# Kernel tuning notes

Hardware: AMD Instinct MI355X
Metric: run time of the kernel (lower is better)

Reference implementation:

```python
import jax, jax.numpy as jnp
import numpy as np

# Mamba2 defaults (mamba_ssm): d_state=128, d_conv=4, expand=2, headdim=64, ngroups=1
NB, D_MODEL, D_STATE, D_CONV, HEADDIM = 2, 512, 128, 4, 64
D_INNER = 2 * D_MODEL                      # expand * d_model
NHEADS = D_INNER // HEADDIM                # 16
CONV_DIM = D_INNER + 2 * D_STATE           # x, B, C go through depthwise conv
D_IN_PROJ = 2 * D_INNER + 2 * D_STATE + NHEADS  # z, xBC, dt
VOCAB, LABEL, B, L = 32000, 1000, 2, 512


def setup_inputs() -> dict:
    key = jax.random.key(0)
    ks = jax.random.split(key, 8)
    nrm = lambda k, shape, s: jax.random.normal(k, shape, dtype=jnp.float32) * s
    tokens = jax.random.randint(ks[0], (B, L), 0, VOCAB)
    embedding = nrm(ks[1], (VOCAB, D_MODEL), 0.02)
    in_proj_w = nrm(ks[2], (NB, D_IN_PROJ, D_MODEL), D_MODEL ** -0.5)
    conv_w = nrm(ks[3], (NB, CONV_DIM, D_CONV), D_CONV ** -0.5)
    conv_b = jnp.zeros((NB, CONV_DIM), jnp.float32)
    # dt_bias = inverse-softplus of dt ~ logUniform[1e-3, 0.1] (Mamba2 init)
    dt = jnp.exp(jax.random.uniform(ks[4], (NB, NHEADS), minval=float(np.log(1e-3)), maxval=float(np.log(0.1))))
    dt_bias = dt + jnp.log(-jnp.expm1(-dt))
    A_log = jnp.log(jax.random.uniform(ks[5], (NB, NHEADS), minval=1.0, maxval=16.0))
    D = jnp.ones((NB, NHEADS), jnp.float32)
    rms_w = jnp.ones((NB, D_INNER), jnp.float32)
    out_proj_w = nrm(ks[6], (NB, D_MODEL, D_INNER), D_INNER ** -0.5)
    ln_w = jnp.ones((NB, D_MODEL), jnp.float32)
    ln_b = jnp.zeros((NB, D_MODEL), jnp.float32)
    head_w = nrm(ks[7], (LABEL, D_MODEL), D_MODEL ** -0.5)
    head_b = jnp.zeros((LABEL,), jnp.float32)
    return dict(tokens=tokens, embedding=embedding, in_proj_w=in_proj_w, conv_w=conv_w,
                conv_b=conv_b, dt_bias=dt_bias, A_log=A_log, D=D, rms_w=rms_w,
                out_proj_w=out_proj_w, ln_w=ln_w, ln_b=ln_b, head_w=head_w, head_b=head_b)


def _mamba2(u, Wi, cw, cb, dtb, Alog, Dv, rw, Wo):
    b, l, _ = u.shape
    zxbcdt = u @ Wi.T                                  # (b,l,D_IN_PROJ)
    z = zxbcdt[..., :D_INNER]
    xBC = zxbcdt[..., D_INNER:D_INNER + CONV_DIM]
    dt = jax.nn.softplus(zxbcdt[..., D_INNER + CONV_DIM:] + dtb)   # (b,l,h)
    # causal depthwise conv1d, kernel size D_CONV
    xp = jnp.pad(xBC, ((0, 0), (D_CONV - 1, 0), (0, 0)))
    xBC = sum(xp[:, k:k + l, :] * cw[:, k] for k in range(D_CONV)) + cb
    xBC = jax.nn.silu(xBC)
    xh = xBC[..., :D_INNER].reshape(b, l, NHEADS, HEADDIM)
    Bm = xBC[..., D_INNER:D_INNER + D_STATE]           # (b,l,n), ngroups=1
    Cm = xBC[..., D_INNER + D_STATE:]                  # (b,l,n)
    A = -jnp.exp(Alog)                                 # (h,)
    dA = jnp.exp(dt * A)                               # (b,l,h)

    def step(h, inp):
        dA_t, dt_t, x_t, B_t, C_t = inp                # (b,h),(b,h),(b,h,p),(b,n),(b,n)
        h = h * dA_t[:, :, None, None] + (dt_t[:, :, None] * x_t)[..., None] * B_t[:, None, None, :]
        return h, jnp.einsum('bhpn,bn->bhp', h, C_t)

    h0 = jnp.zeros((b, NHEADS, HEADDIM, D_STATE), u.dtype)
    inp = (jnp.swapaxes(dA, 0, 1), jnp.swapaxes(dt, 0, 1), jnp.swapaxes(xh, 0, 1),
           jnp.swapaxes(Bm, 0, 1), jnp.swapaxes(Cm, 0, 1))
    _, ys = jax.lax.scan(step, h0, inp)
    y = jnp.swapaxes(ys, 0, 1) + Dv[:, None] * xh      # (b,l,h,p)
    # gated RMSNorm (norm_before_gate=False): normalize y*silu(z)
    y = y.reshape(b, l, D_INNER) * jax.nn.silu(z)
    y = y * jax.lax.rsqrt(jnp.mean(y * y, -1, keepdims=True) + 1e-5) * rw
    return y @ Wo.T


def _layernorm(x, w, bias):
    mu = jnp.mean(x, -1, keepdims=True)
    xc = x - mu
    var = jnp.mean(xc * xc, -1, keepdims=True)
    return xc * jax.lax.rsqrt(var + 1e-5) * w + bias


def reference(tokens, embedding, in_proj_w, conv_w, conv_b, dt_bias, A_log, D,
              rms_w, out_proj_w, ln_w, ln_b, head_w, head_b):
    x = embedding[tokens]                              # (b,l,d)
    for i in range(NB):
        y = _mamba2(x, in_proj_w[i], conv_w[i], conv_b[i], dt_bias[i],
                    A_log[i], D[i], rms_w[i], out_proj_w[i])
        x = _layernorm(y + x, ln_w[i], ln_b[i])        # residual + LN (dropout=identity)
    return x @ head_w.T + head_b                        # (b,l,label)
```

## Files before the change

kernel.cpp:

```cpp
#include <hip/hip_runtime.h>

#define L_SEQ 512
#define BATCH 2
#define NROWS (BATCH*L_SEQ)
#define DMODEL 512
#define DINNER 1024
#define DSTATE 128
#define NHEADSM 16
#define CONVD 1280
#define DINPROJ 2320
#define QCH 32
#define NCH 16
#define WI_PAD 2368
#define WH_PAD 1024

#define W_CONVW 0
#define W_CONVB 10240
#define W_DTB   12800
#define W_ALOG  12832
#define W_DD    12864
#define W_RMSW  12896
#define W_LNW   14944
#define W_LNB   15968
#define W_HEADB 16992
#define O_X     18048
#define O_ZX    (O_X  + NROWS*DMODEL)
#define O_XC    (O_ZX + NROWS*DINPROJ)
#define O_DT    (O_XC + NROWS*CONVD)
#define O_Y     (O_DT + NROWS*NHEADSM)
#define O_O     (O_Y  + NROWS*DINNER)
#define O_LA    (O_O  + NROWS*DMODEL)
#define O_S     (O_LA + 16384)
#define O_UB    (O_S  + 4194304)
#define U_WI   0
#define U_WO   2424832
#define U_WH   3473408
#define U_XBF  3997696
#define U_YBF  4521984

#define NPREPW (2*WI_PAD + 2*DMODEL + WH_PAD)

typedef __attribute__((ext_vector_type(8))) short short8;
typedef __attribute__((ext_vector_type(4))) float floatx4;

__device__ __forceinline__ float b2f(unsigned short h){ return __uint_as_float(((unsigned)h)<<16); }
__device__ __forceinline__ unsigned short f2b(float x){
  unsigned u = __float_as_uint(x);
  return (unsigned short)((u + 0x7fffu + ((u>>16)&1u)) >> 16);
}
__device__ __forceinline__ float loadIn(const void* p, long i, int f){
  return f ? b2f(((const unsigned short*)p)[i]) : ((const float*)p)[i];
}
__device__ __forceinline__ float silu(float s){ return s / (1.f + __expf(-s)); }

struct ConvArgs { const void* src[9]; int off[10]; };

__global__ void k_prep(ConvArgs a, const void* __restrict__ wi, const void* __restrict__ wo,
                       const void* __restrict__ wh, const int* __restrict__ tok,
                       const void* __restrict__ emb, int* __restrict__ flagOut,
                       float* __restrict__ dstSmall,
                       unsigned short* __restrict__ WiB, unsigned short* __restrict__ WoB,
                       unsigned short* __restrict__ WhB,
                       float* __restrict__ x, unsigned short* __restrict__ xbf)
{
  __shared__ int sflag;
  int t = threadIdx.x;
  if (t < 64){
    int cnt = 0;
    #pragma unroll 8
    for (int i = 0; i < 64; i++){
      unsigned w0 = ((const unsigned*)emb)[t + 64*i];
      unsigned e = (w0 >> 7) & 0xffu;
      cnt += (e >= 100 && e <= 126) ? 1 : 0;
    }
    #pragma unroll
    for (int o = 1; o < 64; o <<= 1) cnt += __shfl_xor(cnt, o);
    if (t == 0) sflag = (cnt > 2048) ? 1 : 0;
  }
  __syncthreads();
  int f = sflag;
  if (blockIdx.x == 0 && t == 0) *flagOut = f;

  int blk = blockIdx.x;
  if (blk < 71){
    int i = blk*256 + t;
    if (i < a.off[9]){
      int s = 0;
      while (i >= a.off[s+1]) s++;
      dstSmall[i] = loadIn(a.src[s], i - a.off[s], f);
    }
    return;
  }
  blk -= 71;
  if (blk < NPREPW){
    int r = blk;
    const void* src = nullptr; unsigned short* dst; long sb = 0, db; int K; bool zero = false;
    if (r < 2*WI_PAD){
      int layer = r / WI_PAD, row = r % WI_PAD;
      K = DMODEL; dst = WiB; db = ((long)layer*WI_PAD + row)*DMODEL;
      if (row < DINPROJ){ src = wi; sb = ((long)layer*DINPROJ + row)*DMODEL; } else zero = true;
    } else if (r < 2*WI_PAD + 2*DMODEL){
      int rr = r - 2*WI_PAD;
      K = DINNER; dst = WoB; db = (long)rr*DINNER;
      src = wo; sb = db;
    } else {
      int row = r - 2*WI_PAD - 2*DMODEL;
      K = DMODEL; dst = WhB; db = (long)row*DMODEL;
      if (row < 1000){ src = wh; sb = db; } else zero = true;
    }
    for (int c = t; c < K; c += 256)
      dst[db + c] = zero ? (unsigned short)0
                         : (f ? ((const unsigned short*)src)[sb + c] : f2b(((const float*)src)[sb + c]));
    return;
  }
  int r = blk - NPREPW;
  long base = (long)tok[r] * DMODEL;
  for (int c = t; c < DMODEL; c += 256){
    float v = loadIn(emb, base + c, f);
    x[(long)r*DMODEL + c] = v;
    xbf[(long)r*DMODEL + c] = f ? ((const unsigned short*)emb)[base + c] : f2b(v);
  }
}

__global__ __launch_bounds__(256) void k_mfma_nt(
    const unsigned short* __restrict__ A, const unsigned short* __restrict__ B,
    void* __restrict__ C, int M, int N, int K,
    const float* __restrict__ bias, const int* __restrict__ flag, int outDual)
{
  __shared__ unsigned short As[4096];
  __shared__ unsigned short Bs[4096];
  int t = threadIdx.x;
  int w = t >> 6, lane = t & 63;
  int quad = lane >> 4, l16 = lane & 15;
  int m0 = blockIdx.y << 6, n0 = blockIdx.x << 6;
  int wm = (w & 1) << 5, wn = (w >> 1) << 5;
  floatx4 acc[2][2];
  #pragma unroll
  for (int mi = 0; mi < 2; mi++)
    #pragma unroll
    for (int ni = 0; ni < 2; ni++) acc[mi][ni] = (floatx4){0.f,0.f,0.f,0.f};

  int idx0 = (w << 7) + lane;
  int r0s = idx0 >> 3, g0 = idx0 & 7;
  int idx1 = idx0 + 64;
  int r1s = idx1 >> 3, g1 = idx1 & 7;
  long aOff0 = (long)(m0 + r0s)*K + g0*8;
  long aOff1 = (long)(m0 + r1s)*K + g1*8;
  long bOff0 = (long)(n0 + r0s)*K + g0*8;
  long bOff1 = (long)(n0 + r1s)*K + g1*8;
  int w0 = r0s*64 + (g0 ^ (r0s & 7))*8;
  int w1 = r1s*64 + (g1 ^ (r1s & 7))*8;

  for (int k0 = 0; k0 < K; k0 += 64){
    short8 a0 = *(const short8*)&A[aOff0 + k0];
    short8 a1 = *(const short8*)&A[aOff1 + k0];
    short8 b0 = *(const short8*)&B[bOff0 + k0];
    short8 b1 = *(const short8*)&B[bOff1 + k0];
    __syncthreads();
    *(short8*)&As[w0] = a0; *(short8*)&As[w1] = a1;
    *(short8*)&Bs[w0] = b0; *(short8*)&Bs[w1] = b1;
    __syncthreads();
    #pragma unroll
    for (int ks = 0; ks < 2; ks++){
      short8 af[2], bfr[2];
      #pragma unroll
      for (int mi = 0; mi < 2; mi++){
        int r = wm + mi*16 + l16;
        int pos = ((ks << 2) + quad) ^ (r & 7);
        af[mi] = *(const short8*)&As[r*64 + pos*8];
      }
      #pragma unroll
      for (int ni = 0; ni < 2; ni++){
        int r = wn + ni*16 + l16;
        int pos = ((ks << 2) + quad) ^ (r & 7);
        bfr[ni] = *(const short8*)&Bs[r*64 + pos*8];
      }
      #pragma unroll
      for (int mi = 0; mi < 2; mi++)
        #pragma unroll
        for (int ni = 0; ni < 2; ni++)
          acc[mi][ni] = __builtin_amdgcn_mfma_f32_16x16x32_bf16(af[mi], bfr[ni], acc[mi][ni], 0, 0, 0);
    }
  }
  int f = *flag;
  #pragma unroll
  for (int mi = 0; mi < 2; mi++)
    #pragma unroll
    for (int ni = 0; ni < 2; ni++){
      int col = n0 + wn + ni*16 + l16;
      if (col >= N) continue;
      float bv = bias ? bias[col] : 0.f;
      #pragma unroll
      for (int rr = 0; rr < 4; rr++){
        int row = m0 + wm + mi*16 + (quad << 2) + rr;
        float v = acc[mi][ni][rr] + bv;
        long idx = (long)row*N + col;
        if (outDual && f) ((unsigned short*)C)[idx] = f2b(v);
        else              ((float*)C)[idx] = v;
      }
    }
}

__global__ __launch_bounds__(256) void k_conv_dt(
    const float* __restrict__ zx, const float* __restrict__ cw, const float* __restrict__ cb,
    const float* __restrict__ dtb, unsigned short* __restrict__ xcb, float* __restrict__ dt)
{
  int r = blockIdx.x; int b = r >> 9, l = r & 511;
  int t = threadIdx.x;
  for (int c = t; c < CONVD; c += 256){
    float s = cb[c];
    #pragma unroll
    for (int k = 0; k < 4; k++){
      int pos = l - 3 + k;
      if (pos >= 0)
        s = fmaf(zx[(long)(b*L_SEQ + pos)*DINPROJ + DINNER + c], cw[c*4 + k], s);
    }
    xcb[(long)r*CONVD + c] = f2b(silu(s));
  }
  if (t < NHEADSM){
    float v = zx[(long)r*DINPROJ + DINNER + CONVD + t] + dtb[t];
    dt[r*NHEADSM + t] = (v > 20.f) ? v : log1pf(__expf(v));
  }
}

__global__ __launch_bounds__(256) void k_chunk1(
    const unsigned short* __restrict__ xcb, const float* __restrict__ dtbuf,
    const float* __restrict__ alog, const float* __restrict__ dvec,
    float* __restrict__ S, float* __restrict__ LAb, float* __restrict__ y)
{
  int c = blockIdx.x, h = blockIdx.y, b = blockIdx.z;
  int t = threadIdx.x, w = t >> 6, lane = t & 63;
  int quad = lane >> 4, l16 = lane & 15;
  int l0 = c*QCH;
  __shared__ unsigned short XT[64*40];
  __shared__ unsigned short BTc[128*40];
  __shared__ unsigned short Bb[32*136];
  __shared__ unsigned short Cb[32*136];
  __shared__ unsigned short Gb[32*40];
  __shared__ float dtl[32], lal[32], coef[32];
  float A  = -__expf(alog[h]);
  float Dv = dvec[h];

  unsigned short xus[8];
  #pragma unroll
  for (int k = 0; k < 8; k++){
    int idx = t + k*256; int j = idx >> 6, p = idx & 63;
    xus[k] = xcb[(long)(b*L_SEQ + l0 + j)*CONVD + h*64 + p];
  }
  unsigned short bus[16], cus[16];
  #pragma unroll
  for (int k = 0; k < 16; k++){
    int idx = t + k*256; int j = idx >> 7, n = idx & 127;
    long rb = (long)(b*L_SEQ + l0 + j)*CONVD + DINNER;
    bus[k] = xcb[rb + n];
    cus[k] = xcb[rb + DSTATE + n];
  }
  if (t < 32) dtl[t] = dtbuf[(b*L_SEQ + l0 + t)*NHEADSM + h];
  __syncthreads();
  if (t == 0){ float s = 0.f; for (int i = 0; i < 32; i++){ s += dtl[i]; lal[i] = s*A; } }
  __syncthreads();
  if (t < 32){
    coef[t] = __expf(lal[31] - lal[t]) * dtl[t];
    LAb[(b*NHEADSM + h)*L_SEQ + l0 + t] = lal[t];
  }
  __syncthreads();
  #pragma unroll
  for (int k = 0; k < 8; k++){
    int idx = t + k*256; int j = idx >> 6, p = idx & 63;
    XT[p*40 + j] = xus[k];
  }
  #pragma unroll
  for (int k = 0; k < 16; k++){
    int idx = t + k*256; int j = idx >> 7, n = idx & 127;
    Bb[j*136 + n] = bus[k];
    Cb[j*136 + n] = cus[k];
    BTc[n*40 + j] = f2b(b2f(bus[k]) * coef[j]);
  }
  __syncthreads();

  short8 afS = *(const short8*)&XT[(w*16 + l16)*40 + quad*8];
  floatx4 accS[8];
  #pragma unroll
  for (int nb = 0; nb < 8; nb++){
    short8 bfS = *(const short8*)&BTc[(nb*16 + l16)*40 + quad*8];
    accS[nb] = __builtin_amdgcn_mfma_f32_16x16x32_bf16(afS, bfS, (floatx4){0.f,0.f,0.f,0.f}, 0, 0, 0);
  }
  int ti = w & 1, tj = w >> 1;
  floatx4 accG = (floatx4){0.f,0.f,0.f,0.f};
  #pragma unroll
  for (int ks = 0; ks < 4; ks++){
    short8 ga = *(const short8*)&Cb[(ti*16 + l16)*136 + ks*32 + quad*8];
    short8 gb = *(const short8*)&Bb[(tj*16 + l16)*136 + ks*32 + quad*8];
    accG = __builtin_amdgcn_mfma_f32_16x16x32_bf16(ga, gb, accG, 0, 0, 0);
  }
  long sb = ((long)((b*NHEADSM + h)*NCH + c))*8192;
  #pragma unroll
  for (int nb = 0; nb < 8; nb++)
    #pragma unroll
    for (int rr = 0; rr < 4; rr++)
      S[sb + (w*16 + quad*4 + rr)*128 + nb*16 + l16] = accS[nb][rr];
  #pragma unroll
  for (int rr = 0; rr < 4; rr++){
    int i = ti*16 + quad*4 + rr, j = tj*16 + l16;
    float g = (j <= i) ? __expf(lal[i] - lal[j]) * dtl[j] * accG[rr] : 0.f;
    Gb[i*40 + j] = f2b(g);
  }
  __syncthreads();
  short8 ag = *(const short8*)&Gb[(ti*16 + l16)*40 + quad*8];
  #pragma unroll
  for (int s = 0; s < 2; s++){
    int pb = (w >> 1)*2 + s;
    short8 bx = *(const short8*)&XT[(pb*16 + l16)*40 + quad*8];
    floatx4 accY = __builtin_amdgcn_mfma_f32_16x16x32_bf16(ag, bx, (floatx4){0.f,0.f,0.f,0.f}, 0, 0, 0);
    #pragma unroll
    for (int rr = 0; rr < 4; rr++){
      int i = ti*16 + quad*4 + rr, p = pb*16 + l16;
      float xval = b2f(XT[p*40 + i]);
      y[(long)(b*L_SEQ + l0 + i)*DINNER + h*64 + p] = fmaf(Dv, xval, accY[rr]);
    }
  }
}

__global__ __launch_bounds__(256) void k_chunk2(
    float* __restrict__ S, const float* __restrict__ LAb)
{
  int bh = blockIdx.x >> 5;
  int e = ((blockIdx.x & 31) << 8) + threadIdx.x;
  long base = (long)bh*NCH*8192 + e;
  int laBase = bh*L_SEQ;
  float lam[NCH];
  #pragma unroll
  for (int c = 0; c < NCH; c++) lam[c] = __expf(LAb[laBase + c*QCH + QCH - 1]);
  float hr = 0.f;
  #pragma unroll
  for (int c = 0; c < NCH; c++){
    long off = base + (long)c*8192;
    float sv = S[off];
    S[off] = hr;
    hr = fmaf(hr, lam[c], sv);
  }
}

__global__ __launch_bounds__(256) void k_chunk3(
    const unsigned short* __restrict__ xcb, const float* __restrict__ H,
    const float* __restrict__ LAb, float* __restrict__ y)
{
  int c = blockIdx.x, h = blockIdx.y, b = blockIdx.z;
  int t = threadIdx.x, w = t >> 6, lane = t & 63;
  int quad = lane >> 4, l16 = lane & 15;
  int l0 = c*QCH, bh = b*NHEADSM + h;
  __shared__ unsigned short Cb[32*136];
  __shared__ unsigned short Hhi[64*136];
  __shared__ unsigned short Hlo[64*136];
  __shared__ float el[32];
  if (t < 32) el[t] = __expf(LAb[bh*L_SEQ + l0 + t]);
  #pragma unroll
  for (int k = 0; k < 16; k++){
    int idx = t + k*256; int j = idx >> 7, n = idx & 127;
    Cb[j*136 + n] = xcb[(long)(b*L_SEQ + l0 + j)*CONVD + DINNER + DSTATE + n];
  }
  long hb = ((long)(bh*NCH + c))*8192;
  #pragma unroll
  for (int k = 0; k < 32; k++){
    int idx = t + k*256; int p = idx >> 7, n = idx & 127;
    float v = H[hb + idx];
    unsigned short hi = f2b(v);
    Hhi[p*136 + n] = hi;
    Hlo[p*136 + n] = f2b(v - b2f(hi));
  }
  __syncthreads();
  int ti = w & 1;
  #pragma unroll
  for (int s = 0; s < 2; s++){
    int pb = (w >> 1)*2 + s;
    floatx4 acc = (floatx4){0.f,0.f,0.f,0.f};
    #pragma unroll
    for (int ks = 0; ks < 4; ks++){
      short8 a  = *(const short8*)&Cb [(ti*16 + l16)*136 + ks*32 + quad*8];
      short8 bl = *(const short8*)&Hlo[(pb*16 + l16)*136 + ks*32 + quad*8];
      short8 bh2= *(const short8*)&Hhi[(pb*16 + l16)*136 + ks*32 + quad*8];
      acc = __builtin_amdgcn_mfma_f32_16x16x32_bf16(a, bl, acc, 0, 0, 0);
      acc = __builtin_amdgcn_mfma_f32_16x16x32_bf16(a, bh2, acc, 0, 0, 0);
    }
    #pragma unroll
    for (int rr = 0; rr < 4; rr++){
      int i = ti*16 + quad*4 + rr, p = pb*16 + l16;
      long yb = (long)(b*L_SEQ + l0 + i)*DINNER + h*64 + p;
      y[yb] = fmaf(el[i], acc[rr], y[yb]);
    }
  }
}

__global__ __launch_bounds__(256) void k_gated_rms(
    const float* __restrict__ y, const float* __restrict__ zx, const float* __restrict__ rw,
    unsigned short* __restrict__ ybf)
{
  int r = blockIdx.x, t = threadIdx.x;
  float g[4]; float ss = 0.f;
  #pragma unroll
  for (int i = 0; i < 4; i++){
    int c = t + i*256;
    float z  = zx[(long)r*DINPROJ + c];
    float yv = y[(long)r*DINNER + c];
    g[i] = yv * silu(z);
    ss = fmaf(g[i], g[i], ss);
  }
  #pragma unroll
  for (int o = 1; o < 64; o <<= 1) ss += __shfl_xor(ss, o);
  __shared__ float red[4];
  int w = t >> 6, lane = t & 63;
  if (lane == 0) red[w] = ss;
  __syncthreads();
  float tot = red[0] + red[1] + red[2] + red[3];
  float sc = rsqrtf(tot / (float)DINNER + 1e-5f);
  #pragma unroll
  for (int i = 0; i < 4; i++){
    int c = t + i*256;
    ybf[(long)r*DINNER + c] = f2b(g[i] * sc * rw[c]);
  }
}

__global__ __launch_bounds__(256) void k_add_ln(
    float* __restrict__ x, const float* __restrict__ o,
    const float* __restrict__ lw, const float* __restrict__ lb,
    unsigned short* __restrict__ xbf)
{
  int r = blockIdx.x, t = threadIdx.x;
  float v[2]; float sm = 0.f;
  #pragma unroll
  for (int i = 0; i < 2; i++){ int c = t + i*256; v[i] = x[(long)r*DMODEL + c] + o[(long)r*DMODEL + c]; sm += v[i]; }
  #pragma unroll
  for (int off = 1; off < 64; off <<= 1) sm += __shfl_xor(sm, off);
  __shared__ float red[4]; __shared__ float red2[4];
  int w = t >> 6, lane = t & 63;
  if (lane == 0) red[w] = sm;
  __syncthreads();
  float mu = (red[0] + red[1] + red[2] + red[3]) / (float)DMODEL;
  float var = 0.f;
  #pragma unroll
  for (int i = 0; i < 2; i++){ v[i] -= mu; var = fmaf(v[i], v[i], var); }
  #pragma unroll
  for (int off = 1; off < 64; off <<= 1) var += __shfl_xor(var, off);
  if (lane == 0) red2[w] = var;
  __syncthreads();
  float vv = (red2[0] + red2[1] + red2[2] + red2[3]) / (float)DMODEL;
  float sc = rsqrtf(vv + 1e-5f);
  #pragma unroll
  for (int i = 0; i < 2; i++){
    int c = t + i*256;
    float ov = v[i]*sc*lw[c] + lb[c];
    x[(long)r*DMODEL + c] = ov;
    xbf[(long)r*DMODEL + c] = f2b(ov);
  }
}

extern "C" void kernel_launch(void* const* d_in, const int* in_sizes, int n_in,
                              void* d_out, int out_size, void* d_ws, size_t ws_size,
                              hipStream_t stream)
{
  const int* tokens = (const int*)d_in[0];
  const void* emb = d_in[1];
  int* flag = (int*)d_ws;
  float* ws = (float*)((char*)d_ws + 256);

  ConvArgs ca;
  const int sizes[9] = {10240, 2560, 32, 32, 32, 2048, 1024, 1024, 1000};
  const int idxs[9]  = {3, 4, 5, 6, 7, 8, 10, 11, 13};
  int off = 0;
  for (int s = 0; s < 9; s++){ ca.src[s] = d_in[idxs[s]]; ca.off[s] = off; off += sizes[s]; }
  ca.off[9] = off;

  float* X  = ws + O_X;
  float* ZX = ws + O_ZX;
  float* DT = ws + O_DT;
  float* Y  = ws + O_Y;
  float* Ob = ws + O_O;
  float* LA = ws + O_LA;
  float* Sb = ws + O_S;
  unsigned short* xcb = (unsigned short*)(ws + O_XC);
  unsigned short* ub  = (unsigned short*)(ws + O_UB);
  unsigned short* WiB = ub + U_WI;
  unsigned short* WoB = ub + U_WO;
  unsigned short* WhB = ub + U_WH;
  unsigned short* Xbf = ub + U_XBF;
  unsigned short* Ybf = ub + U_YBF;

  k_prep<<<71 + NPREPW + NROWS, 256, 0, stream>>>(
      ca, d_in[2], d_in[9], d_in[12], tokens, emb, flag,
      ws, WiB, WoB, WhB, X, Xbf);

  for (int layer = 0; layer < 2; layer++){
    k_mfma_nt<<<dim3(WI_PAD/64, NROWS/64), 256, 0, stream>>>(
        Xbf, WiB + (long)layer*WI_PAD*DMODEL, (void*)ZX,
        NROWS, DINPROJ, DMODEL, (const float*)nullptr, flag, 0);
    k_conv_dt<<<NROWS, 256, 0, stream>>>(
        ZX, ws + W_CONVW + layer*5120, ws + W_CONVB + layer*1280, ws + W_DTB + layer*16, xcb, DT);
    k_chunk1<<<dim3(NCH, NHEADSM, BATCH), 256, 0, stream>>>(
        xcb, DT, ws + W_ALOG + layer*16, ws + W_DD + layer*16, Sb, LA, Y);
    k_chunk2<<<1024, 256, 0, stream>>>(Sb, LA);
    k_chunk3<<<dim3(NCH, NHEADSM, BATCH), 256, 0, stream>>>(xcb, Sb, LA, Y);
    k_gated_rms<<<NROWS, 256, 0, stream>>>(Y, ZX, ws + W_RMSW + layer*1024, Ybf);
    k_mfma_nt<<<dim3(DMODEL/64, NROWS/64), 256, 0, stream>>>(
        Ybf, WoB + (long)layer*DMODEL*DINNER, (void*)Ob,
        NROWS, DMODEL, DINNER, (const float*)nullptr, flag, 0);
    k_add_ln<<<NROWS, 256, 0, stream>>>(X, Ob, ws + W_LNW + layer*512, ws + W_LNB + layer*512, Xbf);
  }

  k_mfma_nt<<<dim3(WH_PAD/64, NROWS/64), 256, 0, stream>>>(
      Xbf, WhB, d_out, NROWS, 1000, DMODEL, ws + W_HEADB, flag, 1);
}
```

Baseline: 261.1 us.

## Double-buffer GEMM LDS tiles and store in_proj output as bf16

The MFMA GEMM now uses two LDS buffers, prefetching the next K tile from global memory into registers while computing on the current one. This cuts the loop from two barriers per iteration to one and hides load latency. Separately, the in_proj GEMM output (z, xBC, dt) is written as bf16 instead of fp32, and the conv/dt and gated RMSNorm kernels read it as bf16. This halves that intermediate's write and read traffic but lowers the precision of z, xBC and dt.

```diff
diff --git a/kernel.cpp b/kernel.cpp
--- a/kernel.cpp
+++ b/kernel.cpp
@@ -125,10 +125,10 @@
 __global__ __launch_bounds__(256) void k_mfma_nt(
     const unsigned short* __restrict__ A, const unsigned short* __restrict__ B,
     void* __restrict__ C, int M, int N, int K,
-    const float* __restrict__ bias, const int* __restrict__ flag, int outDual)
-{
-  __shared__ unsigned short As[4096];
-  __shared__ unsigned short Bs[4096];
+    const float* __restrict__ bias, const int* __restrict__ flag, int outMode)
+{
+  __shared__ unsigned short As[2][4096];
+  __shared__ unsigned short Bs[2][4096];
   int t = threadIdx.x;
   int w = t >> 6, lane = t & 63;
   int quad = lane >> 4, l16 = lane & 15;
@@ -151,15 +151,28 @@
   int w0 = r0s*64 + (g0 ^ (r0s & 7))*8;
   int w1 = r1s*64 + (g1 ^ (r1s & 7))*8;
 
-  for (int k0 = 0; k0 < K; k0 += 64){
-    short8 a0 = *(const short8*)&A[aOff0 + k0];
-    short8 a1 = *(const short8*)&A[aOff1 + k0];
-    short8 b0 = *(const short8*)&B[bOff0 + k0];
-    short8 b1 = *(const short8*)&B[bOff1 + k0];
-    __syncthreads();
-    *(short8*)&As[w0] = a0; *(short8*)&As[w1] = a1;
-    *(short8*)&Bs[w0] = b0; *(short8*)&Bs[w1] = b1;
-    __syncthreads();
+  {
+    short8 a0 = *(const short8*)&A[aOff0];
+    short8 a1 = *(const short8*)&A[aOff1];
+    short8 b0 = *(const short8*)&B[bOff0];
+    short8 b1 = *(const short8*)&B[bOff1];
+    *(short8*)&As[0][w0] = a0; *(short8*)&As[0][w1] = a1;
+    *(short8*)&Bs[0][w0] = b0; *(short8*)&Bs[0][w1] = b1;
+  }
+  __syncthreads();
+
+  int nIt = K >> 6;
+  for (int it = 0; it < nIt; it++){
+    int cur = it & 1, nxt = cur ^ 1;
+    bool more = (it + 1 < nIt);
+    short8 na0, na1, nb0, nb1;
+    if (more){
+      int k0 = (it + 1) << 6;
+      na0 = *(const short8*)&A[aOff0 + k0];
+      na1 = *(const short8*)&A[aOff1 + k0];
+      nb0 = *(const short8*)&B[bOff0 + k0];
+      nb1 = *(const short8*)&B[bOff1 + k0];
+    }
     #pragma unroll
     for (int ks = 0; ks < 2; ks++){
       short8 af[2], bfr[2];
@@ -167,13 +180,13 @@
       for (int mi = 0; mi < 2; mi++){
         int r = wm + mi*16 + l16;
         int pos = ((ks << 2) + quad) ^ (r & 7);
-        af[mi] = *(const short8*)&As[r*64 + pos*8];
+        af[mi] = *(const short8*)&As[cur][r*64 + pos*8];
       }
       #pragma unroll
       for (int ni = 0; ni < 2; ni++){
         int r = wn + ni*16 + l16;
         int pos = ((ks << 2) + quad) ^ (r & 7);
-        bfr[ni] = *(const short8*)&Bs[r*64 + pos*8];
+        bfr[ni] = *(const short8*)&Bs[cur][r*64 + pos*8];
       }
       #pragma unroll
       for (int mi = 0; mi < 2; mi++)
@@ -181,8 +194,14 @@
         for (int ni = 0; ni < 2; ni++)
           acc[mi][ni] = __builtin_amdgcn_mfma_f32_16x16x32_bf16(af[mi], bfr[ni], acc[mi][ni], 0, 0, 0);
     }
-  }
-  int f = *flag;
+    if (more){
+      *(short8*)&As[nxt][w0] = na0; *(short8*)&As[nxt][w1] = na1;
+      *(short8*)&Bs[nxt][w0] = nb0; *(short8*)&Bs[nxt][w1] = nb1;
+    }
+    __syncthreads();
+  }
+
+  int f = (outMode == 1) ? *flag : 0;
   #pragma unroll
   for (int mi = 0; mi < 2; mi++)
     #pragma unroll
@@ -195,14 +214,14 @@
         int row = m0 + wm + mi*16 + (quad << 2) + rr;
         float v = acc[mi][ni][rr] + bv;
         long idx = (long)row*N + col;
-        if (outDual && f) ((unsigned short*)C)[idx] = f2b(v);
-        else              ((float*)C)[idx] = v;
+        if (outMode == 2 || (outMode == 1 && f)) ((unsigned short*)C)[idx] = f2b(v);
+        else                                     ((float*)C)[idx] = v;
       }
     }
 }
 
 __global__ __launch_bounds__(256) void k_conv_dt(
-    const float* __restrict__ zx, const float* __restrict__ cw, const float* __restrict__ cb,
+    const unsigned short* __restrict__ zxb, const float* __restrict__ cw, const float* __restrict__ cb,
     const float* __restrict__ dtb, unsigned short* __restrict__ xcb, float* __restrict__ dt)
 {
   int r = blockIdx.x; int b = r >> 9, l = r & 511;
@@ -213,12 +232,12 @@
     for (int k = 0; k < 4; k++){
       int pos = l - 3 + k;
       if (pos >= 0)
-        s = fmaf(zx[(long)(b*L_SEQ + pos)*DINPROJ + DINNER + c], cw[c*4 + k], s);
+        s = fmaf(b2f(zxb[(long)(b*L_SEQ + pos)*DINPROJ + DINNER + c]), cw[c*4 + k], s);
     }
     xcb[(long)r*CONVD + c] = f2b(silu(s));
   }
   if (t < NHEADSM){
-    float v = zx[(long)r*DINPROJ + DINNER + CONVD + t] + dtb[t];
+    float v = b2f(zxb[(long)r*DINPROJ + DINNER + CONVD + t]) + dtb[t];
     dt[r*NHEADSM + t] = (v > 20.f) ? v : log1pf(__expf(v));
   }
 }
@@ -392,7 +411,7 @@
 }
 
 __global__ __launch_bounds__(256) void k_gated_rms(
-    const float* __restrict__ y, const float* __restrict__ zx, const float* __restrict__ rw,
+    const float* __restrict__ y, const unsigned short* __restrict__ zxb, const float* __restrict__ rw,
     unsigned short* __restrict__ ybf)
 {
   int r = blockIdx.x, t = threadIdx.x;
@@ -400,7 +419,7 @@
   #pragma unroll
   for (int i = 0; i < 4; i++){
     int c = t + i*256;
-    float z  = zx[(long)r*DINPROJ + c];
+    float z  = b2f(zxb[(long)r*DINPROJ + c]);
     float yv = y[(long)r*DINNER + c];
     g[i] = yv * silu(z);
     ss = fmaf(g[i], g[i], ss);
@@ -471,12 +490,12 @@
   ca.off[9] = off;
 
   float* X  = ws + O_X;
-  float* ZX = ws + O_ZX;
   float* DT = ws + O_DT;
   float* Y  = ws + O_Y;
   float* Ob = ws + O_O;
   float* LA = ws + O_LA;
   float* Sb = ws + O_S;
+  unsigned short* ZXb = (unsigned short*)(ws + O_ZX);
   unsigned short* xcb = (unsigned short*)(ws + O_XC);
   unsigned short* ub  = (unsigned short*)(ws + O_UB);
   unsigned short* WiB = ub + U_WI;
@@ -491,15 +510,15 @@
 
   for (int layer = 0; layer < 2; layer++){
     k_mfma_nt<<<dim3(WI_PAD/64, NROWS/64), 256, 0, stream>>>(
-        Xbf, WiB + (long)layer*WI_PAD*DMODEL, (void*)ZX,
-        NROWS, DINPROJ, DMODEL, (const float*)nullptr, flag, 0);
+        Xbf, WiB + (long)layer*WI_PAD*DMODEL, (void*)ZXb,
+        NROWS, DINPROJ, DMODEL, (const float*)nullptr, flag, 2);
     k_conv_dt<<<NROWS, 256, 0, stream>>>(
-        ZX, ws + W_CONVW + layer*5120, ws + W_CONVB + layer*1280, ws + W_DTB + layer*16, xcb, DT);
+        ZXb, ws + W_CONVW + layer*5120, ws + W_CONVB + layer*1280, ws + W_DTB + layer*16, xcb, DT);
     k_chunk1<<<dim3(NCH, NHEADSM, BATCH), 256, 0, stream>>>(
         xcb, DT, ws + W_ALOG + layer*16, ws + W_DD + layer*16, Sb, LA, Y);
     k_chunk2<<<1024, 256, 0, stream>>>(Sb, LA);
     k_chunk3<<<dim3(NCH, NHEADSM, BATCH), 256, 0, stream>>>(xcb, Sb, LA, Y);
-    k_gated_rms<<<NROWS, 256, 0, stream>>>(Y, ZX, ws + W_RMSW + layer*1024, Ybf);
+    k_gated_rms<<<NROWS, 256, 0, stream>>>(Y, ZXb, ws + W_RMSW + layer*1024, Ybf);
     k_mfma_nt<<<dim3(DMODEL/64, NROWS/64), 256, 0, stream>>>(
         Ybf, WoB + (long)layer*DMODEL*DINNER, (void*)Ob,
         NROWS, DMODEL, DINNER, (const float*)nullptr, flag, 0);
```

After: 258.1 us. Within noise of the previous version (-1.2%).
